# Kernel optimization log

Measured on AMD Instinct MI355X. Metric: run time of the kernel, lower is better.

Reference implementation:

```python
import jax, jax.numpy as jnp
import numpy as np

DIM = 1024
N_HEADS = 16
HEAD = DIM // N_HEADS
MLP = 4096


def layer_norm(x, g, b, eps=1e-5):
    mu = jnp.mean(x, axis=-1, keepdims=True)
    var = jnp.mean(jnp.square(x - mu), axis=-1, keepdims=True)
    return (x - mu) * jax.lax.rsqrt(var + eps) * g + b


def setup_inputs() -> dict:
    key = jax.random.key(0)
    ks = jax.random.split(key, 12)
    s = 0.02
    return {
        "x": jax.random.normal(ks[0], (4, 1024, DIM), dtype=jnp.float32),
        "Wq": jax.random.normal(ks[1], (DIM, DIM), dtype=jnp.float32) * s,
        "Wk": jax.random.normal(ks[2], (DIM, DIM), dtype=jnp.float32) * s,
        "Wv": jax.random.normal(ks[3], (DIM, DIM), dtype=jnp.float32) * s,
        "Wo": jax.random.normal(ks[4], (DIM, DIM), dtype=jnp.float32) * s,
        "W1": jax.random.normal(ks[5], (DIM, MLP), dtype=jnp.float32) * s,
        "b1": jnp.zeros((MLP,), dtype=jnp.float32),
        "W2": jax.random.normal(ks[6], (MLP, DIM), dtype=jnp.float32) * s,
        "b2": jnp.zeros((DIM,), dtype=jnp.float32),
        "g_ln1": jnp.ones((DIM,), dtype=jnp.float32),
        "b_ln1": jnp.zeros((DIM,), dtype=jnp.float32),
        "g_ln2": jnp.ones((DIM,), dtype=jnp.float32),
        "b_ln2": jnp.zeros((DIM,), dtype=jnp.float32),
    }


def reference(x, Wq, Wk, Wv, Wo, W1, b1, W2, b2, g_ln1, b_ln1, g_ln2, b_ln2):
    b, l, _ = x.shape
    # --- attention sublayer with pre-LN residual ---
    h = layer_norm(x, g_ln1, b_ln1)
    q = (h @ Wq).reshape(b, N_HEADS, l, HEAD)  # faithful to torch .view (no transpose)
    k = (h @ Wk).reshape(b, N_HEADS, l, HEAD)
    v = (h @ Wv).reshape(b, N_HEADS, l, HEAD)
    scores = jnp.einsum('bnid,bnjd->bnij', q, k) / np.float32(HEAD ** 0.5)
    w = jax.nn.softmax(scores, axis=-1)
    o = jnp.einsum('bnij,bnjd->bnid', w, v)
    o = o.transpose(0, 2, 1, 3).reshape(b, l, DIM)  # 'b n i d -> b i (n d)'
    x = x + o @ Wo
    # --- FFN sublayer with pre-LN residual (exact GELU) ---
    h2 = layer_norm(x, g_ln2, b_ln2)
    f = jax.nn.gelu(h2 @ W1 + b1, approximate=False) @ W2 + b2
    return x + f
```

## Files before the change

kernel.cpp:

```cpp
#include <hip/hip_runtime.h>
#include <math.h>

#define DIM 1024
#define SEQ 1024
#define BATCH 4
#define NHEADS 16
#define HEADD 64
#define MLP_DIM 4096

typedef short short8 __attribute__((ext_vector_type(8)));
typedef float f32x4 __attribute__((ext_vector_type(4)));
#define MFMA(a, b, c) __builtin_amdgcn_mfma_f32_16x16x32_bf16(a, b, c, 0, 0, 0)

__device__ __forceinline__ ushort f2b(float x) {
  unsigned u = __float_as_uint(x);
  unsigned r = (u + 0x7FFFu + ((u >> 16) & 1u)) >> 16;
  return (ushort)r;
}
__device__ __forceinline__ float b2f(ushort h) {
  return __uint_as_float(((unsigned)h) << 16);
}

__device__ __forceinline__ void g2l16(const void* g, void* l) {
  __builtin_amdgcn_global_load_lds((const __attribute__((address_space(1))) void*)g,
                                   (__attribute__((address_space(3))) void*)l, 16, 0, 0);
}

__device__ __forceinline__ void xcd_swz(int& bx, int& by) {
  int gx = gridDim.x;
  int id = blockIdx.x + gx * blockIdx.y;
  int cpx = (gx * gridDim.y) >> 3;
  int sid = (id & 7) * cpx + (id >> 3);
  bx = sid % gx;
  by = sid / gx;
}

__device__ __forceinline__ void cvt8(const float* f, float scale, short8& hi, short8& lo) {
#pragma unroll
  for (int i = 0; i < 8; i++) {
    float v = f[i] * scale;
    ushort hv = f2b(v);
    hi[i] = (short)hv;
    lo[i] = (short)f2b(v - b2f(hv));
  }
}

__global__ __launch_bounds__(256) void ln_kernel(const float* __restrict__ x,
                                                 const float* __restrict__ g,
                                                 const float* __restrict__ b,
                                                 ushort* __restrict__ ohi,
                                                 ushort* __restrict__ olo) {
  int row = blockIdx.x;
  int t = threadIdx.x;
  const float* xr = x + (size_t)row * DIM;
  float4 v = *(const float4*)(xr + t * 4);
  float s  = v.x + v.y + v.z + v.w;
  float sq = v.x * v.x + v.y * v.y + v.z * v.z + v.w * v.w;
#pragma unroll
  for (int off = 32; off > 0; off >>= 1) {
    s  += __shfl_down(s, off);
    sq += __shfl_down(sq, off);
  }
  __shared__ float red_s[4], red_q[4];
  __shared__ float mu_s, inv_s;
  int wid = t >> 6;
  if ((t & 63) == 0) { red_s[wid] = s; red_q[wid] = sq; }
  __syncthreads();
  if (t == 0) {
    float S  = red_s[0] + red_s[1] + red_s[2] + red_s[3];
    float Sq = red_q[0] + red_q[1] + red_q[2] + red_q[3];
    float mu  = S * (1.0f / DIM);
    float var = Sq * (1.0f / DIM) - mu * mu;
    mu_s  = mu;
    inv_s = 1.0f / sqrtf(var + 1e-5f);
  }
  __syncthreads();
  float mu = mu_s, inv = inv_s;
  float4 gv = *(const float4*)(g + t * 4);
  float4 bv = *(const float4*)(b + t * 4);
  float o0 = (v.x - mu) * inv * gv.x + bv.x;
  float o1 = (v.y - mu) * inv * gv.y + bv.y;
  float o2 = (v.z - mu) * inv * gv.z + bv.z;
  float o3 = (v.w - mu) * inv * gv.w + bv.w;
  ushort4 hv, lv;
  hv.x = f2b(o0); lv.x = f2b(o0 - b2f(hv.x));
  hv.y = f2b(o1); lv.y = f2b(o1 - b2f(hv.y));
  hv.z = f2b(o2); lv.z = f2b(o2 - b2f(hv.z));
  hv.w = f2b(o3); lv.w = f2b(o3 - b2f(hv.w));
  *(ushort4*)(ohi + (size_t)row * DIM + t * 4) = hv;
  *(ushort4*)(olo + (size_t)row * DIM + t * 4) = lv;
}

__global__ __launch_bounds__(256) void wprep_kernel(const float* __restrict__ W,
                                                    ushort* __restrict__ Whi,
                                                    ushort* __restrict__ Wlo,
                                                    int Kd, int Nd) {
  __shared__ float tile[64][65];
  const int t = threadIdx.x;
  const int n0 = blockIdx.x * 64, k0 = blockIdx.y * 64;
  const int r = t >> 4, c4 = (t & 15) * 4;
#pragma unroll
  for (int i = 0; i < 4; i++) {
    float4 v = *(const float4*)&W[(size_t)(k0 + r + i * 16) * Nd + n0 + c4];
    tile[r + i * 16][c4 + 0] = v.x;
    tile[r + i * 16][c4 + 1] = v.y;
    tile[r + i * 16][c4 + 2] = v.z;
    tile[r + i * 16][c4 + 3] = v.w;
  }
  __syncthreads();
#pragma unroll
  for (int i = 0; i < 4; i++) {
    int nr = r + i * 16;
    float x0 = tile[c4 + 0][nr], x1 = tile[c4 + 1][nr];
    float x2 = tile[c4 + 2][nr], x3 = tile[c4 + 3][nr];
    ushort4 hv, lv;
    hv.x = f2b(x0); lv.x = f2b(x0 - b2f(hv.x));
    hv.y = f2b(x1); lv.y = f2b(x1 - b2f(hv.y));
    hv.z = f2b(x2); lv.z = f2b(x2 - b2f(hv.z));
    hv.w = f2b(x3); lv.w = f2b(x3 - b2f(hv.w));
    *(ushort4*)&Whi[(size_t)(n0 + nr) * Kd + k0 + c4] = hv;
    *(ushort4*)&Wlo[(size_t)(n0 + nr) * Kd + k0 + c4] = lv;
  }
}

template <int MS, int NS, int EPI>
__device__ __forceinline__ void mgemm_body(
    const ushort* __restrict__ Ahi, const ushort* __restrict__ Alo,
    const ushort* __restrict__ Bhi, const ushort* __restrict__ Blo,
    const float* __restrict__ bias, const float* __restrict__ res,
    float* __restrict__ Cf, ushort* __restrict__ Chi, ushort* __restrict__ Clo,
    int M, int N, int K) {
  constexpr int ASUB = 2 * MS;
  constexpr int BSUB = 2 * NS;
  constexpr int TOT = 2 * (ASUB + BSUB);
  constexpr int PW = TOT / 4;
  __shared__ ushort lds[TOT * 512];

  int bx, by;
  xcd_swz(bx, by);
  const int t = threadIdx.x;
  const int l = t & 63;
  const int wid = t >> 6;
  const int wm = wid >> 1, wn = wid & 1;
  const int m0 = by * (ASUB * 16);
  const int n0 = bx * (BSUB * 16);
  const int lr = l & 15;
  const int lk = (l >> 4) * 8;

  const ushort* gsrc[PW];
  ushort* ldst[PW];
#pragma unroll
  for (int i = 0; i < PW; i++) {
    int j = wid * PW + i;
    const ushort* base;
    int rowbase, slot;
    if (j < 2 * ASUB) {
      int plane = j & 1, sub = j >> 1;
      base = plane ? Alo : Ahi;
      rowbase = m0 + sub * 16;
      slot = plane * ASUB + sub;
    } else {
      int jb = j - 2 * ASUB;
      int plane = jb & 1, sub = jb >> 1;
      base = plane ? Blo : Bhi;
      rowbase = n0 + sub * 16;
      slot = 2 * ASUB + plane * BSUB + sub;
    }
    gsrc[i] = base + (size_t)(rowbase + lr) * K + lk;
    ldst[i] = &lds[slot * 512];
  }

  f32x4 acc[MS][NS] = {};

  for (int k0 = 0; k0 < K; k0 += 32) {
    __syncthreads();
#pragma unroll
    for (int i = 0; i < PW; i++) {
      g2l16(gsrc[i], ldst[i]);
      gsrc[i] += 32;
    }
    __syncthreads();

    short8 ah[MS], al[MS], bh[NS], bl[NS];
#pragma unroll
    for (int mi = 0; mi < MS; mi++) {
      ah[mi] = *(const short8*)&lds[(wm * MS + mi) * 512 + l * 8];
      al[mi] = *(const short8*)&lds[(ASUB + wm * MS + mi) * 512 + l * 8];
    }
#pragma unroll
    for (int ni = 0; ni < NS; ni++) {
      bh[ni] = *(const short8*)&lds[(2 * ASUB + wn * NS + ni) * 512 + l * 8];
      bl[ni] = *(const short8*)&lds[(2 * ASUB + BSUB + wn * NS + ni) * 512 + l * 8];
    }
#pragma unroll
    for (int mi = 0; mi < MS; mi++)
#pragma unroll
      for (int ni = 0; ni < NS; ni++) {
        acc[mi][ni] = MFMA(ah[mi], bh[ni], acc[mi][ni]);
        acc[mi][ni] = MFMA(ah[mi], bl[ni], acc[mi][ni]);
        acc[mi][ni] = MFMA(al[mi], bh[ni], acc[mi][ni]);
      }
  }

  const int orow0 = m0 + wm * (MS * 16);
  const int ocol0 = n0 + wn * (NS * 16);
#pragma unroll
  for (int mi = 0; mi < MS; mi++) {
#pragma unroll
    for (int r = 0; r < 4; r++) {
      int row = orow0 + mi * 16 + (l >> 4) * 4 + r;
#pragma unroll
      for (int ni = 0; ni < NS; ni++) {
        int col = ocol0 + ni * 16 + lr;
        size_t idx = (size_t)row * N + col;
        float v = acc[mi][ni][r];
        if (EPI == 0) {
          Cf[idx] = v;
        } else if (EPI == 1) {
          Cf[idx] = v + res[idx];
        } else if (EPI == 2) {
          v += bias[col];
          v = 0.5f * v * (1.0f + erff(v * 0.70710678118654752f));
          ushort h = f2b(v);
          Chi[idx] = h;
          Clo[idx] = f2b(v - b2f(h));
        } else {
          Cf[idx] = v + bias[col] + res[idx];
        }
      }
    }
  }
}

template <int MS, int NS, int EPI, int MINW>
__global__ __launch_bounds__(256, MINW) void mgemm_kernel(
    const ushort* __restrict__ Ahi, const ushort* __restrict__ Alo,
    const ushort* __restrict__ Bhi, const ushort* __restrict__ Blo,
    const float* __restrict__ bias, const float* __restrict__ res,
    float* __restrict__ Cf, ushort* __restrict__ Chi, ushort* __restrict__ Clo,
    int M, int N, int K) {
  mgemm_body<MS, NS, EPI>(Ahi, Alo, Bhi, Blo, bias, res, Cf, Chi, Clo, M, N, K);
}

__global__ __launch_bounds__(256, 2) void qkv_mfma(
    const ushort* __restrict__ Ahi, const ushort* __restrict__ Alo,
    const ushort* __restrict__ Wqh, const ushort* __restrict__ Wql,
    const ushort* __restrict__ Wkh, const ushort* __restrict__ Wkl,
    const ushort* __restrict__ Wvh, const ushort* __restrict__ Wvl,
    float* __restrict__ Qo, float* __restrict__ Ko, float* __restrict__ Vo) {
  const ushort* bh = (blockIdx.z == 0) ? Wqh : (blockIdx.z == 1) ? Wkh : Wvh;
  const ushort* bl = (blockIdx.z == 0) ? Wql : (blockIdx.z == 1) ? Wkl : Wvl;
  float* C = (blockIdx.z == 0) ? Qo : (blockIdx.z == 1) ? Ko : Vo;
  mgemm_body<4, 4, 0>(Ahi, Alo, bh, bl, nullptr, nullptr, C, nullptr, nullptr,
                      4096, DIM, DIM);
}

#define KSLOT(s, ks, pl) (((s) * 2 + (ks)) * 1024 + (pl) * 512)
#define VSLOT(d, ks, pl) (8192 + ((d) * 2 + (ks)) * 1024 + (pl) * 512)
#define PSLOT(w, qf, ks, pl) (16384 + (w) * 4096 + (((qf) * 2 + (ks)) * 2 + (pl)) * 512)

__global__ __launch_bounds__(256, 2) void attn_mfma(const float* __restrict__ Q,
                                                    const float* __restrict__ K,
                                                    const float* __restrict__ V,
                                                    ushort* __restrict__ Ohi,
                                                    ushort* __restrict__ Olo) {
  __shared__ ushort lds[32768];
  const int qt = blockIdx.x;
  const int n  = blockIdx.y;
  const int bi = blockIdx.z;
  const size_t headoff = ((size_t)bi * SEQ + (size_t)n * HEADD) * DIM;
  const float* Qh = Q + headoff;
  const float* Kh = K + headoff;
  const float* Vh = V + headoff;
  const int t = threadIdx.x;
  const int l = t & 63;
  const int w = t >> 6;
  const int lq = l & 15;
  const int h = l >> 4;
  const int qrow = qt * 128 + w * 32;

  short8 qfh[2][2], qfl[2][2];
#pragma unroll
  for (int qf = 0; qf < 2; qf++) {
    const float* qp = Qh + (size_t)(qrow + qf * 16 + lq) * 64 + h * 8;
#pragma unroll
    for (int ks = 0; ks < 2; ks++) {
      float f[8];
      float4 a = *(const float4*)(qp + ks * 32);
      float4 b = *(const float4*)(qp + ks * 32 + 4);
      f[0]=a.x; f[1]=a.y; f[2]=a.z; f[3]=a.w; f[4]=b.x; f[5]=b.y; f[6]=b.z; f[7]=b.w;
      cvt8(f, 1.0f, qfh[qf][ks], qfl[qf][ks]);
    }
  }

  f32x4 accO[4][2] = {};
  float m_run[2] = {-1e30f, -1e30f};
  float l_run[2] = {0.0f, 0.0f};

  for (int tdx = 0; tdx < SEQ / 64; tdx++) {
    const int kvbase = tdx * 64;
    __syncthreads();
    {
      const float* kp = Kh + (size_t)(kvbase + 16 * w + lq) * 64 + h * 8;
#pragma unroll
      for (int ks = 0; ks < 2; ks++) {
        float f[8];
        float4 a = *(const float4*)(kp + ks * 32);
        float4 b = *(const float4*)(kp + ks * 32 + 4);
        f[0]=a.x; f[1]=a.y; f[2]=a.z; f[3]=a.w; f[4]=b.x; f[5]=b.y; f[6]=b.z; f[7]=b.w;
        short8 hi, lo;
        cvt8(f, 0.125f, hi, lo);
        *(short8*)&lds[KSLOT(w, ks, 0) + l * 8] = hi;
        *(short8*)&lds[KSLOT(w, ks, 1) + l * 8] = lo;
      }
    }
    {
#pragma unroll
      for (int ks = 0; ks < 2; ks++) {
        float f[8];
#pragma unroll
        for (int j = 0; j < 8; j++)
          f[j] = Vh[(size_t)(kvbase + ks * 32 + h * 8 + j) * 64 + 16 * w + lq];
        short8 hi, lo;
        cvt8(f, 1.0f, hi, lo);
        *(short8*)&lds[VSLOT(w, ks, 0) + l * 8] = hi;
        *(short8*)&lds[VSLOT(w, ks, 1) + l * 8] = lo;
      }
    }
    __syncthreads();

    f32x4 accS[4][2] = {};
#pragma unroll
    for (int ks = 0; ks < 2; ks++) {
      short8 kh[4], kl[4];
#pragma unroll
      for (int s = 0; s < 4; s++) {
        kh[s] = *(const short8*)&lds[KSLOT(s, ks, 0) + l * 8];
        kl[s] = *(const short8*)&lds[KSLOT(s, ks, 1) + l * 8];
      }
#pragma unroll
      for (int s = 0; s < 4; s++)
#pragma unroll
        for (int qf = 0; qf < 2; qf++) {
          accS[s][qf] = MFMA(kh[s], qfh[qf][ks], accS[s][qf]);
          accS[s][qf] = MFMA(kh[s], qfl[qf][ks], accS[s][qf]);
          accS[s][qf] = MFMA(kl[s], qfh[qf][ks], accS[s][qf]);
        }
    }

    float corr[2];
#pragma unroll
    for (int qf = 0; qf < 2; qf++) {
      float tmax = -1e30f;
#pragma unroll
      for (int s = 0; s < 4; s++)
#pragma unroll
        for (int r = 0; r < 4; r++) tmax = fmaxf(tmax, accS[s][qf][r]);
      tmax = fmaxf(tmax, __shfl_xor(tmax, 16));
      tmax = fmaxf(tmax, __shfl_xor(tmax, 32));
      float mnew = fmaxf(m_run[qf], tmax);
      float c = __expf(m_run[qf] - mnew);
      m_run[qf] = mnew;
      corr[qf] = c;
      float tsum = 0.0f;
#pragma unroll
      for (int s = 0; s < 4; s++)
#pragma unroll
        for (int r = 0; r < 4; r++) {
          float p = __expf(accS[s][qf][r] - mnew);
          accS[s][qf][r] = p;
          tsum += p;
        }
      tsum += __shfl_xor(tsum, 16);
      tsum += __shfl_xor(tsum, 32);
      l_run[qf] = l_run[qf] * c + tsum;
    }

#pragma unroll
    for (int qf = 0; qf < 2; qf++)
#pragma unroll
      for (int s = 0; s < 4; s++) {
        f32x4 p = accS[s][qf];
        ushort4 hv, lv;
        hv.x = f2b(p[0]); lv.x = f2b(p[0] - b2f(hv.x));
        hv.y = f2b(p[1]); lv.y = f2b(p[1] - b2f(hv.y));
        hv.z = f2b(p[2]); lv.z = f2b(p[2] - b2f(hv.z));
        hv.w = f2b(p[3]); lv.w = f2b(p[3] - b2f(hv.w));
        int ib = (((s & 1) * 2) + (h >> 1)) * 128 + lq * 8 + (h & 1) * 4;
        *(ushort4*)&lds[PSLOT(w, qf, s >> 1, 0) + ib] = hv;
        *(ushort4*)&lds[PSLOT(w, qf, s >> 1, 1) + ib] = lv;
      }

#pragma unroll
    for (int df = 0; df < 4; df++)
#pragma unroll
      for (int qf = 0; qf < 2; qf++)
#pragma unroll
        for (int r = 0; r < 4; r++) accO[df][qf][r] *= corr[qf];

#pragma unroll
    for (int ks = 0; ks < 2; ks++) {
      short8 vh[4], vl[4], ph[2], pl[2];
#pragma unroll
      for (int d = 0; d < 4; d++) {
        vh[d] = *(const short8*)&lds[VSLOT(d, ks, 0) + l * 8];
        vl[d] = *(const short8*)&lds[VSLOT(d, ks, 1) + l * 8];
      }
#pragma unroll
      for (int qf = 0; qf < 2; qf++) {
        ph[qf] = *(const short8*)&lds[PSLOT(w, qf, ks, 0) + l * 8];
        pl[qf] = *(const short8*)&lds[PSLOT(w, qf, ks, 1) + l * 8];
      }
#pragma unroll
      for (int d = 0; d < 4; d++)
#pragma unroll
        for (int qf = 0; qf < 2; qf++) {
          accO[d][qf] = MFMA(vh[d], ph[qf], accO[d][qf]);
          accO[d][qf] = MFMA(vl[d], ph[qf], accO[d][qf]);
          accO[d][qf] = MFMA(vh[d], pl[qf], accO[d][qf]);
        }
    }
  }

#pragma unroll
  for (int qf = 0; qf < 2; qf++) {
    float inv = 1.0f / l_run[qf];
    int qg = qrow + qf * 16 + lq;
    size_t base = ((size_t)bi * SEQ + qg) * DIM + n * HEADD;
#pragma unroll
    for (int df = 0; df < 4; df++) {
      f32x4 o = accO[df][qf];
      float v0 = o[0] * inv, v1 = o[1] * inv, v2 = o[2] * inv, v3 = o[3] * inv;
      ushort4 hv, lv;
      hv.x = f2b(v0); lv.x = f2b(v0 - b2f(hv.x));
      hv.y = f2b(v1); lv.y = f2b(v1 - b2f(hv.y));
      hv.z = f2b(v2); lv.z = f2b(v2 - b2f(hv.z));
      hv.w = f2b(v3); lv.w = f2b(v3 - b2f(hv.w));
      size_t a = base + df * 16 + h * 4;
      *(ushort4*)(Ohi + a) = hv;
      *(ushort4*)(Olo + a) = lv;
    }
  }
}

extern "C" void kernel_launch(void* const* d_in, const int* in_sizes, int n_in,
                              void* d_out, int out_size, void* d_ws, size_t ws_size,
                              hipStream_t stream) {
  const float* x    = (const float*)d_in[0];
  const float* Wq   = (const float*)d_in[1];
  const float* Wk   = (const float*)d_in[2];
  const float* Wv   = (const float*)d_in[3];
  const float* Wo   = (const float*)d_in[4];
  const float* W1   = (const float*)d_in[5];
  const float* b1   = (const float*)d_in[6];
  const float* W2   = (const float*)d_in[7];
  const float* b2   = (const float*)d_in[8];
  const float* gln1 = (const float*)d_in[9];
  const float* bln1 = (const float*)d_in[10];
  const float* gln2 = (const float*)d_in[11];
  const float* bln2 = (const float*)d_in[12];
  float* out = (float*)d_out;
  char* W = (char*)d_ws;

  const size_t MB = 1u << 20;
  ushort* Wqh = (ushort*)(W + 0 * MB);
  ushort* Wql = (ushort*)(W + 2 * MB);
  ushort* Wkh = (ushort*)(W + 4 * MB);
  ushort* Wkl = (ushort*)(W + 6 * MB);
  ushort* Wvh = (ushort*)(W + 8 * MB);
  ushort* Wvl = (ushort*)(W + 10 * MB);
  ushort* Woh = (ushort*)(W + 12 * MB);
  ushort* Wol = (ushort*)(W + 14 * MB);
  ushort* W1h = (ushort*)(W + 16 * MB);
  ushort* W1l = (ushort*)(W + 24 * MB);
  ushort* W2h = (ushort*)(W + 32 * MB);
  ushort* W2l = (ushort*)(W + 40 * MB);
  float*  X2  = (float*) (W + 48 * MB);
  ushort* Hhi = (ushort*)(W + 64 * MB);
  ushort* Hlo = (ushort*)(W + 72 * MB);
  float*  Qb  = (float*) (W + 80 * MB);
  float*  Kb  = (float*) (W + 96 * MB);
  float*  Vb  = (float*) (W + 112 * MB);
  ushort* F1h = (ushort*)(W + 80 * MB);
  ushort* F1l = (ushort*)(W + 112 * MB);
  ushort* Ohi = (ushort*)(W + 128 * MB);
  ushort* Olo = (ushort*)(W + 136 * MB);

  wprep_kernel<<<dim3(16, 16), 256, 0, stream>>>(Wq, Wqh, Wql, DIM, DIM);
  wprep_kernel<<<dim3(16, 16), 256, 0, stream>>>(Wk, Wkh, Wkl, DIM, DIM);
  wprep_kernel<<<dim3(16, 16), 256, 0, stream>>>(Wv, Wvh, Wvl, DIM, DIM);
  wprep_kernel<<<dim3(16, 16), 256, 0, stream>>>(Wo, Woh, Wol, DIM, DIM);
  wprep_kernel<<<dim3(64, 16), 256, 0, stream>>>(W1, W1h, W1l, DIM, MLP_DIM);
  wprep_kernel<<<dim3(16, 64), 256, 0, stream>>>(W2, W2h, W2l, MLP_DIM, DIM);
  ln_kernel<<<4096, 256, 0, stream>>>(x, gln1, bln1, Hhi, Hlo);
  qkv_mfma<<<dim3(8, 32, 3), 256, 0, stream>>>(Hhi, Hlo, Wqh, Wql, Wkh, Wkl,
                                               Wvh, Wvl, Qb, Kb, Vb);
  attn_mfma<<<dim3(8, 16, 4), 256, 0, stream>>>(Qb, Kb, Vb, Ohi, Olo);
  mgemm_kernel<2, 4, 1, 4><<<dim3(8, 64), 256, 0, stream>>>(
      Ohi, Olo, Woh, Wol, nullptr, x, X2, nullptr, nullptr, 4096, DIM, DIM);
  ln_kernel<<<4096, 256, 0, stream>>>(X2, gln2, bln2, Hhi, Hlo);
  mgemm_kernel<4, 4, 2, 2><<<dim3(32, 32), 256, 0, stream>>>(
      Hhi, Hlo, W1h, W1l, b1, nullptr, nullptr, F1h, F1l, 4096, MLP_DIM, DIM);
  mgemm_kernel<2, 4, 3, 4><<<dim3(8, 64), 256, 0, stream>>>(
      F1h, F1l, W2h, W2l, b2, X2, out, nullptr, nullptr, 4096, DIM, MLP_DIM);
}
```

Measured before the change: 715.0 us.

## Split-K the Wo and W2 GEMMs in two with a separate reduction kernel

The Wo projection and W2 FFN GEMMs, which previously launched 512 blocks each, now split the K dimension in half across blockIdx.z. This doubles the block count to improve occupancy across the CUs. Each half writes an fp32 partial into scratch buffers that reuse workspace regions. A new elementwise kernel then sums the two partials with the residual and optional bias. In exchange the change adds extra global-memory traffic for the partials, two more kernel launches, and a risk of aliasing if the reused workspace regions are still live.

New measurement: 741.1 us. 3.7% more time.

```diff
diff --git a/kernel.cpp b/kernel.cpp
--- a/kernel.cpp
+++ b/kernel.cpp
@@ -129,7 +129,7 @@
     const ushort* __restrict__ Bhi, const ushort* __restrict__ Blo,
     const float* __restrict__ bias, const float* __restrict__ res,
     float* __restrict__ Cf, ushort* __restrict__ Chi, ushort* __restrict__ Clo,
-    int M, int N, int K) {
+    int M, int N, int Klen, int Kstride, int Koff) {
   constexpr int ASUB = 2 * MS;
   constexpr int BSUB = 2 * NS;
   constexpr int TOT = 2 * (ASUB + BSUB);
@@ -166,13 +166,13 @@
       rowbase = n0 + sub * 16;
       slot = 2 * ASUB + plane * BSUB + sub;
     }
-    gsrc[i] = base + (size_t)(rowbase + lr) * K + lk;
+    gsrc[i] = base + (size_t)(rowbase + lr) * Kstride + Koff + lk;
     ldst[i] = &lds[slot * 512];
   }
 
   f32x4 acc[MS][NS] = {};
 
-  for (int k0 = 0; k0 < K; k0 += 32) {
+  for (int k0 = 0; k0 < Klen; k0 += 32) {
     __syncthreads();
 #pragma unroll
     for (int i = 0; i < PW; i++) {
@@ -239,7 +239,42 @@
     const float* __restrict__ bias, const float* __restrict__ res,
     float* __restrict__ Cf, ushort* __restrict__ Chi, ushort* __restrict__ Clo,
     int M, int N, int K) {
-  mgemm_body<MS, NS, EPI>(Ahi, Alo, Bhi, Blo, bias, res, Cf, Chi, Clo, M, N, K);
+  mgemm_body<MS, NS, EPI>(Ahi, Alo, Bhi, Blo, bias, res, Cf, Chi, Clo,
+                          M, N, K, K, 0);
+}
+
+template <int MS, int NS, int MINW>
+__global__ __launch_bounds__(256, MINW) void mgemm_sk(
+    const ushort* __restrict__ Ahi, const ushort* __restrict__ Alo,
+    const ushort* __restrict__ Bhi, const ushort* __restrict__ Blo,
+    float* __restrict__ P0, float* __restrict__ P1,
+    int M, int N, int K, int Khalf) {
+  float* P = blockIdx.z ? P1 : P0;
+  mgemm_body<MS, NS, 0>(Ahi, Alo, Bhi, Blo, nullptr, nullptr, P, nullptr,
+                        nullptr, M, N, Khalf, K, blockIdx.z * Khalf);
+}
+
+template <bool BIAS>
+__global__ __launch_bounds__(256) void red2_kernel(const float* __restrict__ P0,
+                                                   const float* __restrict__ P1,
+                                                   const float* __restrict__ bias,
+                                                   const float* __restrict__ res,
+                                                   float* __restrict__ out) {
+  size_t i = (size_t)blockIdx.x * 256 + threadIdx.x;
+  size_t e = i * 4;
+  float4 a = *(const float4*)(P0 + e);
+  float4 b = *(const float4*)(P1 + e);
+  float4 r = *(const float4*)(res + e);
+  float4 o;
+  o.x = a.x + b.x + r.x;
+  o.y = a.y + b.y + r.y;
+  o.z = a.z + b.z + r.z;
+  o.w = a.w + b.w + r.w;
+  if (BIAS) {
+    float4 bb = *(const float4*)(bias + (e & (DIM - 1)));
+    o.x += bb.x; o.y += bb.y; o.z += bb.z; o.w += bb.w;
+  }
+  *(float4*)(out + e) = o;
 }
 
 __global__ __launch_bounds__(256, 2) void qkv_mfma(
@@ -252,7 +287,7 @@
   const ushort* bl = (blockIdx.z == 0) ? Wql : (blockIdx.z == 1) ? Wkl : Wvl;
   float* C = (blockIdx.z == 0) ? Qo : (blockIdx.z == 1) ? Ko : Vo;
   mgemm_body<4, 4, 0>(Ahi, Alo, bh, bl, nullptr, nullptr, C, nullptr, nullptr,
-                      4096, DIM, DIM);
+                      4096, DIM, DIM, DIM, 0);
 }
 
 #define KSLOT(s, ks, pl) (((s) * 2 + (ks)) * 1024 + (pl) * 512)
@@ -485,6 +520,10 @@
   ushort* F1l = (ushort*)(W + 112 * MB);
   ushort* Ohi = (ushort*)(W + 128 * MB);
   ushort* Olo = (ushort*)(W + 136 * MB);
+  float* P0wo = (float*)(W + 64 * MB);
+  float* P1wo = (float*)(W + 80 * MB);
+  float* P0w2 = (float*)(W + 0 * MB);
+  float* P1w2 = (float*)(W + 16 * MB);
 
   wprep_kernel<<<dim3(16, 16), 256, 0, stream>>>(Wq, Wqh, Wql, DIM, DIM);
   wprep_kernel<<<dim3(16, 16), 256, 0, stream>>>(Wk, Wkh, Wkl, DIM, DIM);
@@ -496,11 +535,13 @@
   qkv_mfma<<<dim3(8, 32, 3), 256, 0, stream>>>(Hhi, Hlo, Wqh, Wql, Wkh, Wkl,
                                                Wvh, Wvl, Qb, Kb, Vb);
   attn_mfma<<<dim3(8, 16, 4), 256, 0, stream>>>(Qb, Kb, Vb, Ohi, Olo);
-  mgemm_kernel<2, 4, 1, 4><<<dim3(8, 64), 256, 0, stream>>>(
-      Ohi, Olo, Woh, Wol, nullptr, x, X2, nullptr, nullptr, 4096, DIM, DIM);
+  mgemm_sk<2, 4, 4><<<dim3(8, 64, 2), 256, 0, stream>>>(
+      Ohi, Olo, Woh, Wol, P0wo, P1wo, 4096, DIM, DIM, DIM / 2);
+  red2_kernel<false><<<4096, 256, 0, stream>>>(P0wo, P1wo, nullptr, x, X2);
   ln_kernel<<<4096, 256, 0, stream>>>(X2, gln2, bln2, Hhi, Hlo);
   mgemm_kernel<4, 4, 2, 2><<<dim3(32, 32), 256, 0, stream>>>(
       Hhi, Hlo, W1h, W1l, b1, nullptr, nullptr, F1h, F1l, 4096, MLP_DIM, DIM);
-  mgemm_kernel<2, 4, 3, 4><<<dim3(8, 64), 256, 0, stream>>>(
-      F1h, F1l, W2h, W2l, b2, X2, out, nullptr, nullptr, 4096, DIM, MLP_DIM);
-}
+  mgemm_sk<2, 4, 4><<<dim3(8, 64, 2), 256, 0, stream>>>(
+      F1h, F1l, W2h, W2l, P0w2, P1w2, 4096, DIM, MLP_DIM, MLP_DIM / 2);
+  red2_kernel<true><<<4096, 256, 0, stream>>>(P0w2, P1w2, b2, X2, out);
+}
```
